# Kernel optimization log

Hardware: AMD Instinct MI355X
Metric: run time of the kernel (lower is better)

The kernel has to match this reference:

```python
import jax, jax.numpy as jnp
import numpy as np

N, DIM = 8192, 128
NEG = -1e9  # finite stand-in for -inf; exp underflows to 0 for masked entries


def setup_inputs() -> dict:
    key = jax.random.key(0)
    k1, k2, k3, k4 = jax.random.split(key, 4)
    h = jax.random.normal(k1, (N, DIM), dtype=jnp.float32)
    social_adj = jax.random.randint(k2, (N, N), 0, 2, dtype=jnp.int32)
    # nn.Linear(dim, dim, bias=False): weight [out, in]; xavier-ish scale
    W = jax.random.normal(k3, (DIM, DIM), dtype=jnp.float32) / np.sqrt(DIM)
    a = jax.random.normal(k4, (2 * DIM,), dtype=jnp.float32) / np.sqrt(2 * DIM)
    return {"h": h, "social_adj": social_adj, "W": W, "a": a}


def reference(h, social_adj, W, a):
    Wh = h @ W.T                              # [N, d]
    d = Wh.shape[1]
    a1 = Wh @ a[:d]                           # [N]
    a2 = Wh @ a[d:]                           # [N]
    e = jax.nn.leaky_relu(a1[:, None] + a2[None, :], negative_slope=0.2)  # [N, N]
    mask = social_adj != 0
    e = jnp.where(mask, e, NEG)
    alpha = jax.nn.softmax(e, axis=-1)        # [N, N]
    # rows with no neighbors: torch gives nan->0 via nan_to_num; we zero them directly
    no_neighbor = ~jnp.any(mask, axis=-1)     # [N]
    alpha = jnp.where(no_neighbor[:, None], 0.0, alpha)
    out = alpha @ Wh                          # [N, d]; already 0 on no_neighbor rows
    return out, alpha
```

## Files before the change

### kernel.cpp

```cpp
#include <hip/hip_runtime.h>
#include <hip/hip_bf16.h>

#define NN 8192
#define DIM 128
#define KS 8
#define KSL (NN / KS)
#define RPB 64
#define KC 128

typedef __attribute__((ext_vector_type(8))) short bf16x8;
typedef __attribute__((ext_vector_type(4))) float f32x4;
typedef __attribute__((ext_vector_type(4))) int i32x4;
typedef __attribute__((ext_vector_type(4))) unsigned int u32x4;
typedef __attribute__((ext_vector_type(4))) unsigned short u16x4;
typedef __attribute__((ext_vector_type(4))) short s16x4;

static __device__ inline unsigned short f2bf(float x) {
    __hip_bfloat16 b = __float2bfloat16(x);
    return *reinterpret_cast<unsigned short*>(&b);
}

struct BSplit { short hi, lo; };
static __device__ inline BSplit bsplit(float x) {
    BSplit r;
    __hip_bfloat16 h = __float2bfloat16(x);
    r.hi = *reinterpret_cast<short*>(&h);
    float rem = x - __bfloat162float(h);
    __hip_bfloat16 l = __float2bfloat16(rem);
    r.lo = *reinterpret_cast<short*>(&l);
    return r;
}

__global__ __launch_bounds__(256) void k1m(const float* __restrict__ h,
                                           const float* __restrict__ W,
                                           const float* __restrict__ a,
                                           __hip_bfloat16* __restrict__ whbT,
                                           float* __restrict__ a1g,
                                           unsigned* __restrict__ pku) {
    __shared__ short whi[128 * 132];
    __shared__ short wlo[128 * 132];
    __shared__ short wt[8 * 128 * 8];
    __shared__ float a_sh[256];

    const int tid = threadIdx.x;
    const int wv = tid >> 6, lane = tid & 63;
    const int r0 = blockIdx.x * 64;

    for (int idx = tid; idx < 128 * 128; idx += 256) {
        const int d = idx >> 7, k = idx & 127;
        BSplit s = bsplit(W[idx]);
        whi[d * 132 + k] = s.hi;
        wlo[d * 132 + k] = s.lo;
    }
    a_sh[tid] = a[tid];
    __syncthreads();

    f32x4 acc[8];
    #pragma unroll
    for (int n = 0; n < 8; ++n) acc[n] = (f32x4){0.f, 0.f, 0.f, 0.f};

    const int arow = r0 + wv * 16 + (lane & 15);
    const int ksub = (lane >> 4) * 8;
    const float* hp = h + (size_t)arow * DIM + ksub;

    #pragma unroll
    for (int kk = 0; kk < 128; kk += 32) {
        f32x4 x0 = *(const f32x4*)(hp + kk);
        f32x4 x1 = *(const f32x4*)(hp + kk + 4);
        bf16x8 ah, al;
        {
            BSplit s0 = bsplit(x0.x), s1 = bsplit(x0.y), s2 = bsplit(x0.z), s3 = bsplit(x0.w);
            BSplit s4 = bsplit(x1.x), s5 = bsplit(x1.y), s6 = bsplit(x1.z), s7 = bsplit(x1.w);
            ah[0] = s0.hi; al[0] = s0.lo; ah[1] = s1.hi; al[1] = s1.lo;
            ah[2] = s2.hi; al[2] = s2.lo; ah[3] = s3.hi; al[3] = s3.lo;
            ah[4] = s4.hi; al[4] = s4.lo; ah[5] = s5.hi; al[5] = s5.lo;
            ah[6] = s6.hi; al[6] = s6.lo; ah[7] = s7.hi; al[7] = s7.lo;
        }
        #pragma unroll
        for (int n = 0; n < 8; ++n) {
            const int boff = (n * 16 + (lane & 15)) * 132 + kk + ksub;
            bf16x8 bh = *(const bf16x8*)(whi + boff);
            bf16x8 bl = *(const bf16x8*)(wlo + boff);
            acc[n] = __builtin_amdgcn_mfma_f32_16x16x32_bf16(ah, bh, acc[n], 0, 0, 0);
            acc[n] = __builtin_amdgcn_mfma_f32_16x16x32_bf16(ah, bl, acc[n], 0, 0, 0);
            acc[n] = __builtin_amdgcn_mfma_f32_16x16x32_bf16(al, bh, acc[n], 0, 0, 0);
        }
    }

    float p1[4] = {0.f, 0.f, 0.f, 0.f}, p2[4] = {0.f, 0.f, 0.f, 0.f};
    #pragma unroll
    for (int n = 0; n < 8; ++n) {
        const float av1 = a_sh[n * 16 + (lane & 15)];
        const float av2 = a_sh[128 + n * 16 + (lane & 15)];
        #pragma unroll
        for (int q = 0; q < 4; ++q) {
            p1[q] += acc[n][q] * av1;
            p2[q] += acc[n][q] * av2;
        }
    }
    #pragma unroll
    for (int o = 8; o >= 1; o >>= 1) {
        #pragma unroll
        for (int q = 0; q < 4; ++q) {
            p1[q] += __shfl_xor(p1[q], o, 64);
            p2[q] += __shfl_xor(p2[q], o, 64);
        }
    }
    if ((lane & 15) == 0) {
        #pragma unroll
        for (int q = 0; q < 4; ++q) {
            const int row = r0 + wv * 16 + (lane >> 4) * 4 + q;
            a1g[row] = p1[q];
            const float E1v = expf(p2[q]);
            const float E2v = expf(0.2f * p2[q]);
            pku[row] = (unsigned)f2bf(E1v) | ((unsigned)f2bf(E2v) << 16);
        }
    }

    #pragma unroll
    for (int n = 0; n < 8; ++n) {
        #pragma unroll
        for (int q = 0; q < 4; ++q) {
            const int kloc = wv * 16 + (lane >> 4) * 4 + q;
            const int d = n * 16 + (lane & 15);
            wt[(kloc >> 3) * 1024 + d * 8 + (kloc & 7)] = (short)f2bf(acc[n][q]);
        }
    }
    __syncthreads();
    short* dst = reinterpret_cast<short*>(whbT) + ((size_t)r0 << 7);
    for (int idx = tid * 4; idx < 8192; idx += 1024)
        *(s16x4*)(dst + idx) = *(const s16x4*)(wt + idx);
}

static __device__ inline void sa_group(const i32x4 v, const u32x4 tb,
                                       const float T, const int lane,
                                       float& s1, float& s2,
                                       unsigned* __restrict__ bgrp) {
    unsigned long long m0 = __ballot(v.x != 0);
    unsigned long long m1 = __ballot(v.y != 0);
    unsigned long long m2 = __ballot(v.z != 0);
    unsigned long long m3 = __ballot(v.w != 0);
    if (lane == 0) {
        u32x4 w;
        w.x = (unsigned)m0; w.y = (unsigned)m1;
        w.z = (unsigned)m2; w.w = (unsigned)m3;
        *(u32x4*)(bgrp) = w;
    } else if (lane == 32) {
        u32x4 w;
        w.x = (unsigned)(m0 >> 32); w.y = (unsigned)(m1 >> 32);
        w.z = (unsigned)(m2 >> 32); w.w = (unsigned)(m3 >> 32);
        *(u32x4*)(bgrp + 4) = w;
    }
    float e1, e2; bool px;
    e1 = __uint_as_float(tb.x << 16); e2 = __uint_as_float(tb.x & 0xffff0000u);
    px = (e1 >= T);
    s1 += (v.x && px) ? e1 : 0.f;  s2 += (v.x && !px) ? e2 : 0.f;
    e1 = __uint_as_float(tb.y << 16); e2 = __uint_as_float(tb.y & 0xffff0000u);
    px = (e1 >= T);
    s1 += (v.y && px) ? e1 : 0.f;  s2 += (v.y && !px) ? e2 : 0.f;
    e1 = __uint_as_float(tb.z << 16); e2 = __uint_as_float(tb.z & 0xffff0000u);
    px = (e1 >= T);
    s1 += (v.z && px) ? e1 : 0.f;  s2 += (v.z && !px) ? e2 : 0.f;
    e1 = __uint_as_float(tb.w << 16); e2 = __uint_as_float(tb.w & 0xffff0000u);
    px = (e1 >= T);
    s1 += (v.w && px) ? e1 : 0.f;  s2 += (v.w && !px) ? e2 : 0.f;
}

__global__ __launch_bounds__(256) void sa_scan(const int* __restrict__ adj,
                                               const float* __restrict__ a1g,
                                               const unsigned* __restrict__ pku,
                                               unsigned* __restrict__ bm,
                                               float* __restrict__ crow) {
    const int wid = threadIdx.x >> 6, lane = threadIdx.x & 63;
    const int i = blockIdx.x * 4 + wid;
    const float a1i = a1g[i];
    const float T = expf(-a1i);
    const int* arow = adj + (size_t)i * NN;
    unsigned* brow = bm + (size_t)i * (NN / 32);

    float s1 = 0.f, s2 = 0.f;
    for (int it = 0; it < NN / 1024; ++it) {
        const int j0 = it * 1024 + lane * 4;
        i32x4 v0 = __builtin_nontemporal_load((const i32x4*)(arow + j0));
        i32x4 v1 = __builtin_nontemporal_load((const i32x4*)(arow + j0 + 256));
        i32x4 v2 = __builtin_nontemporal_load((const i32x4*)(arow + j0 + 512));
        i32x4 v3 = __builtin_nontemporal_load((const i32x4*)(arow + j0 + 768));
        u32x4 t0 = *(const u32x4*)(pku + j0);
        u32x4 t1 = *(const u32x4*)(pku + j0 + 256);
        u32x4 t2 = *(const u32x4*)(pku + j0 + 512);
        u32x4 t3 = *(const u32x4*)(pku + j0 + 768);
        unsigned* bsup = brow + it * 32;
        sa_group(v0, t0, T, lane, s1, s2, bsup);
        sa_group(v1, t1, T, lane, s1, s2, bsup + 8);
        sa_group(v2, t2, T, lane, s1, s2, bsup + 16);
        sa_group(v3, t3, T, lane, s1, s2, bsup + 24);
    }
    #pragma unroll
    for (int o = 32; o >= 1; o >>= 1) {
        s1 += __shfl_xor(s1, o, 64);
        s2 += __shfl_xor(s2, o, 64);
    }
    if (lane == 0) {
        float c1 = 0.f, c2 = 0.f;
        if (s1 + s2 > 0.f) {
            float e1v = expf(a1i);
            float e2v = expf(0.2f * a1i);
            float S = e1v * s1 + e2v * s2;
            c1 = e1v / S;
            c2 = e2v / S;
        }
        crow[i * 4 + 0] = c1;
        crow[i * 4 + 1] = c2;
        crow[i * 4 + 2] = T;
        crow[i * 4 + 3] = 0.f;
    }
}

__global__ __launch_bounds__(512, 8) void sb_pv(const unsigned* __restrict__ bm,
                                                const float* __restrict__ crowG,
                                                const unsigned* __restrict__ pku,
                                                const __hip_bfloat16* __restrict__ whbT,
                                                float* __restrict__ alpha,
                                                float* __restrict__ part) {
    __shared__ __hip_bfloat16 abuf[2][RPB][KC + 8];

    const int tid = threadIdx.x;
    const int wv = tid >> 6, lane = tid & 63;
    const int r0 = blockIdx.x * RPB;
    const int ks = blockIdx.y;
    const int k0 = ks * KSL;

    const int rloc = tid >> 5;
    float c1r[4], c2r[4], Tr[4];
    #pragma unroll
    for (int v = 0; v < 4; ++v) {
        f32x4 cw = *(const f32x4*)(crowG + (size_t)(r0 + rloc + 16 * v) * 4);
        c1r[v] = cw.x; c2r[v] = cw.y; Tr[v] = cw.z;
    }

    f32x4 acc[4];
    #pragma unroll
    for (int rt = 0; rt < 4; ++rt) acc[rt] = (f32x4){0.f, 0.f, 0.f, 0.f};
    const int n0 = wv * 16;
    const short* wb = reinterpret_cast<const short*>(whbT);
    const short* bbase = wb + (size_t)(n0 + (lane & 15)) * 8 + (size_t)(lane >> 4) * 1024;

    const int cgrp = (tid & 31) << 2;
    const unsigned pbit = tid & 31;

    for (int kc = 0; kc < KSL; kc += KC) {
        const int dbuf = (kc >> 7) & 1;
        const int jl = kc + cgrp;
        const int j = k0 + jl;
        const int wbw = ((jl >> 8) << 3) + (((jl >> 7) & 1) << 2);
        u32x4 tb = *(const u32x4*)(pku + j);
        float e1c[4], e2c[4];
        e1c[0] = __uint_as_float(tb.x << 16); e2c[0] = __uint_as_float(tb.x & 0xffff0000u);
        e1c[1] = __uint_as_float(tb.y << 16); e2c[1] = __uint_as_float(tb.y & 0xffff0000u);
        e1c[2] = __uint_as_float(tb.z << 16); e2c[2] = __uint_as_float(tb.z & 0xffff0000u);
        e1c[3] = __uint_as_float(tb.w << 16); e2c[3] = __uint_as_float(tb.w & 0xffff0000u);
        #pragma unroll
        for (int v = 0; v < 4; ++v) {
            const int r = rloc + 16 * v;
            const int gr = r0 + r;
            u32x4 w4 = *(const u32x4*)(bm + (size_t)gr * (NN / 32) + ks * (KSL / 32) + wbw);
            const float c1 = c1r[v], c2 = c2r[v], T = Tr[v];
            f32x4 al;
            al.x = ((w4.x >> pbit) & 1) ? ((e1c[0] >= T) ? c1 * e1c[0] : c2 * e2c[0]) : 0.f;
            al.y = ((w4.y >> pbit) & 1) ? ((e1c[1] >= T) ? c1 * e1c[1] : c2 * e2c[1]) : 0.f;
            al.z = ((w4.z >> pbit) & 1) ? ((e1c[2] >= T) ? c1 * e1c[2] : c2 * e2c[2]) : 0.f;
            al.w = ((w4.w >> pbit) & 1) ? ((e1c[3] >= T) ? c1 * e1c[3] : c2 * e2c[3]) : 0.f;
            __builtin_nontemporal_store(al, (f32x4*)(alpha + (size_t)gr * NN + j));
            u16x4 ub4;
            ub4.x = f2bf(al.x); ub4.y = f2bf(al.y); ub4.z = f2bf(al.z); ub4.w = f2bf(al.w);
            *(u16x4*)(&abuf[dbuf][r][cgrp]) = ub4;
        }
        __syncthreads();
        #pragma unroll
        for (int kk = 0; kk < KC; kk += 32) {
            bf16x8 bf = *(const bf16x8*)(bbase + (size_t)((k0 + kc + kk) >> 3) * 1024);
            #pragma unroll
            for (int rt = 0; rt < 4; ++rt) {
                bf16x8 af = *(const bf16x8*)(&abuf[dbuf][rt * 16 + (lane & 15)][kk + 8 * (lane >> 4)]);
                acc[rt] = __builtin_amdgcn_mfma_f32_16x16x32_bf16(af, bf, acc[rt], 0, 0, 0);
            }
        }
    }

    float* pb2 = part + (size_t)ks * NN * DIM;
    const int rb = (lane >> 4) * 4;
    #pragma unroll
    for (int rt = 0; rt < 4; ++rt) {
        #pragma unroll
        for (int q = 0; q < 4; ++q)
            pb2[(size_t)(r0 + rt * 16 + rb + q) * DIM + n0 + (lane & 15)] = acc[rt][q];
    }
}

__global__ __launch_bounds__(256) void k5_reduce(const float* __restrict__ part,
                                                 float* __restrict__ out) {
    const size_t idx = ((size_t)blockIdx.x * 256 + threadIdx.x) * 4;
    f32x4 s = (f32x4){0.f, 0.f, 0.f, 0.f};
    #pragma unroll
    for (int ks = 0; ks < KS; ++ks)
        s += *(const f32x4*)(part + (size_t)ks * NN * DIM + idx);
    *(f32x4*)(out + idx) = s;
}

extern "C" void kernel_launch(void* const* d_in, const int* in_sizes, int n_in,
                              void* d_out, int out_size, void* d_ws, size_t ws_size,
                              hipStream_t stream) {
    const float* h   = (const float*)d_in[0];
    const int*   adj = (const int*)d_in[1];
    const float* W   = (const float*)d_in[2];
    const float* a   = (const float*)d_in[3];

    float* out   = (float*)d_out;
    float* alpha = out + (size_t)NN * DIM;

    char* ws = (char*)d_ws;
    __hip_bfloat16* whbT = (__hip_bfloat16*)(ws);
    float* a1g    = (float*)(ws + 0x200000);
    unsigned* pku = (unsigned*)(ws + 0x208000);
    float* crow   = (float*)(ws + 0x218000);
    unsigned* bm  = (unsigned*)(ws + 0x240000);
    float* part   = (float*)(ws + 0xA40000);

    k1m<<<NN / 64, 256, 0, stream>>>(h, W, a, whbT, a1g, pku);
    sa_scan<<<NN / 4, 256, 0, stream>>>(adj, a1g, pku, bm, crow);
    sb_pv<<<dim3(NN / RPB, KS), 512, 0, stream>>>(bm, crow, pku, whbT, alpha, part);
    k5_reduce<<<NN * DIM / 1024, 256, 0, stream>>>(part, out);
}
```

Measured before the change: 161.5 us.

## Fuse mask scan, alpha generation and PV matmul into one kernel per 8 rows

Merges the adjacency scan, alpha write/PV MFMA and split-K reduction kernels into a single kernel where each block handles 8 rows. The block keeps the row bitmask and softmax constants in shared memory and accumulates the full K range itself. This removes the global bitmask round trip, the partial-sum buffer and the reduce kernel. In exchange, half of each 16-row MFMA tile is zero padding, so matrix-core work per useful row doubles. Each Wh tile is also reused by only 8 rows, which raises Wh traffic from L2.

```diff
diff --git a/kernel.cpp b/kernel.cpp
--- a/kernel.cpp
+++ b/kernel.cpp
@@ -3,10 +3,8 @@
 
 #define NN 8192
 #define DIM 128
-#define KS 8
-#define KSL (NN / KS)
-#define RPB 64
-#define KC 128
+#define RPB 8
+#define KC 256
 
 typedef __attribute__((ext_vector_type(8))) short bf16x8;
 typedef __attribute__((ext_vector_type(4))) float f32x4;
@@ -135,7 +133,7 @@
 static __device__ inline void sa_group(const i32x4 v, const u32x4 tb,
                                        const float T, const int lane,
                                        float& s1, float& s2,
-                                       unsigned* __restrict__ bgrp) {
+                                       unsigned* bgrp) {
     unsigned long long m0 = __ballot(v.x != 0);
     unsigned long long m1 = __ballot(v.y != 0);
     unsigned long long m2 = __ballot(v.z != 0);
@@ -166,145 +164,103 @@
     s1 += (v.w && px) ? e1 : 0.f;  s2 += (v.w && !px) ? e2 : 0.f;
 }
 
-__global__ __launch_bounds__(256) void sa_scan(const int* __restrict__ adj,
-                                               const float* __restrict__ a1g,
-                                               const unsigned* __restrict__ pku,
-                                               unsigned* __restrict__ bm,
-                                               float* __restrict__ crow) {
-    const int wid = threadIdx.x >> 6, lane = threadIdx.x & 63;
-    const int i = blockIdx.x * 4 + wid;
-    const float a1i = a1g[i];
-    const float T = expf(-a1i);
-    const int* arow = adj + (size_t)i * NN;
-    unsigned* brow = bm + (size_t)i * (NN / 32);
-
-    float s1 = 0.f, s2 = 0.f;
-    for (int it = 0; it < NN / 1024; ++it) {
-        const int j0 = it * 1024 + lane * 4;
-        i32x4 v0 = __builtin_nontemporal_load((const i32x4*)(arow + j0));
-        i32x4 v1 = __builtin_nontemporal_load((const i32x4*)(arow + j0 + 256));
-        i32x4 v2 = __builtin_nontemporal_load((const i32x4*)(arow + j0 + 512));
-        i32x4 v3 = __builtin_nontemporal_load((const i32x4*)(arow + j0 + 768));
-        u32x4 t0 = *(const u32x4*)(pku + j0);
-        u32x4 t1 = *(const u32x4*)(pku + j0 + 256);
-        u32x4 t2 = *(const u32x4*)(pku + j0 + 512);
-        u32x4 t3 = *(const u32x4*)(pku + j0 + 768);
-        unsigned* bsup = brow + it * 32;
-        sa_group(v0, t0, T, lane, s1, s2, bsup);
-        sa_group(v1, t1, T, lane, s1, s2, bsup + 8);
-        sa_group(v2, t2, T, lane, s1, s2, bsup + 16);
-        sa_group(v3, t3, T, lane, s1, s2, bsup + 24);
-    }
-    #pragma unroll
-    for (int o = 32; o >= 1; o >>= 1) {
-        s1 += __shfl_xor(s1, o, 64);
-        s2 += __shfl_xor(s2, o, 64);
-    }
-    if (lane == 0) {
-        float c1 = 0.f, c2 = 0.f;
-        if (s1 + s2 > 0.f) {
-            float e1v = expf(a1i);
-            float e2v = expf(0.2f * a1i);
-            float S = e1v * s1 + e2v * s2;
-            c1 = e1v / S;
-            c2 = e2v / S;
-        }
-        crow[i * 4 + 0] = c1;
-        crow[i * 4 + 1] = c2;
-        crow[i * 4 + 2] = T;
-        crow[i * 4 + 3] = 0.f;
-    }
-}
-
-__global__ __launch_bounds__(512, 8) void sb_pv(const unsigned* __restrict__ bm,
-                                                const float* __restrict__ crowG,
-                                                const unsigned* __restrict__ pku,
-                                                const __hip_bfloat16* __restrict__ whbT,
-                                                float* __restrict__ alpha,
-                                                float* __restrict__ part) {
-    __shared__ __hip_bfloat16 abuf[2][RPB][KC + 8];
+__global__ __launch_bounds__(512, 8) void fs(const int* __restrict__ adj,
+                                             const float* __restrict__ a1g,
+                                             const unsigned* __restrict__ pku,
+                                             const __hip_bfloat16* __restrict__ whbT,
+                                             float* __restrict__ alpha,
+                                             float* __restrict__ out) {
+    __shared__ unsigned bmL[RPB][256];
+    __shared__ __hip_bfloat16 abuf[2][16][KC + 8];
+    __shared__ float crowL[RPB][4];
 
     const int tid = threadIdx.x;
     const int wv = tid >> 6, lane = tid & 63;
     const int r0 = blockIdx.x * RPB;
-    const int ks = blockIdx.y;
-    const int k0 = ks * KSL;
-
-    const int rloc = tid >> 5;
-    float c1r[4], c2r[4], Tr[4];
-    #pragma unroll
-    for (int v = 0; v < 4; ++v) {
-        f32x4 cw = *(const f32x4*)(crowG + (size_t)(r0 + rloc + 16 * v) * 4);
-        c1r[v] = cw.x; c2r[v] = cw.y; Tr[v] = cw.z;
-    }
-
-    f32x4 acc[4];
-    #pragma unroll
-    for (int rt = 0; rt < 4; ++rt) acc[rt] = (f32x4){0.f, 0.f, 0.f, 0.f};
+
+    #pragma unroll
+    for (int b = 0; b < 2; ++b) {
+        unsigned* pz = (unsigned*)&abuf[b][8][0];
+        for (int idx = tid; idx < 4 * (KC + 8); idx += 512) pz[idx] = 0;
+    }
+
+    {
+        const int gi = r0 + wv;
+        const float a1i = a1g[gi];
+        const float T = expf(-a1i);
+        const int* arow = adj + (size_t)gi * NN;
+        float s1 = 0.f, s2 = 0.f;
+        for (int it = 0; it < NN / 512; ++it) {
+            const int j0 = it * 512 + lane * 4;
+            i32x4 v0 = __builtin_nontemporal_load((const i32x4*)(arow + j0));
+            i32x4 v1 = __builtin_nontemporal_load((const i32x4*)(arow + j0 + 256));
+            u32x4 t0 = *(const u32x4*)(pku + j0);
+            u32x4 t1 = *(const u32x4*)(pku + j0 + 256);
+            sa_group(v0, t0, T, lane, s1, s2, &bmL[wv][it * 16]);
+            sa_group(v1, t1, T, lane, s1, s2, &bmL[wv][it * 16 + 8]);
+        }
+        #pragma unroll
+        for (int o = 32; o >= 1; o >>= 1) {
+            s1 += __shfl_xor(s1, o, 64);
+            s2 += __shfl_xor(s2, o, 64);
+        }
+        if (lane == 0) {
+            float c1 = 0.f, c2 = 0.f;
+            if (s1 + s2 > 0.f) {
+                float e1v = expf(a1i);
+                float e2v = expf(0.2f * a1i);
+                float S = e1v * s1 + e2v * s2;
+                c1 = e1v / S;
+                c2 = e2v / S;
+            }
+            crowL[wv][0] = c1; crowL[wv][1] = c2; crowL[wv][2] = T;
+        }
+    }
+    __syncthreads();
+
+    const float c1 = crowL[wv][0], c2 = crowL[wv][1], Tb = crowL[wv][2];
+    f32x4 acc = (f32x4){0.f, 0.f, 0.f, 0.f};
     const int n0 = wv * 16;
     const short* wb = reinterpret_cast<const short*>(whbT);
     const short* bbase = wb + (size_t)(n0 + (lane & 15)) * 8 + (size_t)(lane >> 4) * 1024;
-
-    const int cgrp = (tid & 31) << 2;
-    const unsigned pbit = tid & 31;
-
-    for (int kc = 0; kc < KSL; kc += KC) {
-        const int dbuf = (kc >> 7) & 1;
-        const int jl = kc + cgrp;
-        const int j = k0 + jl;
-        const int wbw = ((jl >> 8) << 3) + (((jl >> 7) & 1) << 2);
+    float* arow_out = alpha + (size_t)(r0 + wv) * NN;
+    const unsigned pbit = lane & 31;
+
+    for (int kc = 0; kc < NN; kc += KC) {
+        const int dbuf = (kc >> 8) & 1;
+        const int j = kc + lane * 4;
+        const int wbw = ((j >> 8) << 3) + (((j >> 7) & 1) << 2);
         u32x4 tb = *(const u32x4*)(pku + j);
+        u32x4 w4 = *(const u32x4*)(&bmL[wv][wbw]);
         float e1c[4], e2c[4];
         e1c[0] = __uint_as_float(tb.x << 16); e2c[0] = __uint_as_float(tb.x & 0xffff0000u);
         e1c[1] = __uint_as_float(tb.y << 16); e2c[1] = __uint_as_float(tb.y & 0xffff0000u);
         e1c[2] = __uint_as_float(tb.z << 16); e2c[2] = __uint_as_float(tb.z & 0xffff0000u);
         e1c[3] = __uint_as_float(tb.w << 16); e2c[3] = __uint_as_float(tb.w & 0xffff0000u);
-        #pragma unroll
-        for (int v = 0; v < 4; ++v) {
-            const int r = rloc + 16 * v;
-            const int gr = r0 + r;
-            u32x4 w4 = *(const u32x4*)(bm + (size_t)gr * (NN / 32) + ks * (KSL / 32) + wbw);
-            const float c1 = c1r[v], c2 = c2r[v], T = Tr[v];
-            f32x4 al;
-            al.x = ((w4.x >> pbit) & 1) ? ((e1c[0] >= T) ? c1 * e1c[0] : c2 * e2c[0]) : 0.f;
-            al.y = ((w4.y >> pbit) & 1) ? ((e1c[1] >= T) ? c1 * e1c[1] : c2 * e2c[1]) : 0.f;
-            al.z = ((w4.z >> pbit) & 1) ? ((e1c[2] >= T) ? c1 * e1c[2] : c2 * e2c[2]) : 0.f;
-            al.w = ((w4.w >> pbit) & 1) ? ((e1c[3] >= T) ? c1 * e1c[3] : c2 * e2c[3]) : 0.f;
-            __builtin_nontemporal_store(al, (f32x4*)(alpha + (size_t)gr * NN + j));
-            u16x4 ub4;
-            ub4.x = f2bf(al.x); ub4.y = f2bf(al.y); ub4.z = f2bf(al.z); ub4.w = f2bf(al.w);
-            *(u16x4*)(&abuf[dbuf][r][cgrp]) = ub4;
-        }
+        f32x4 al;
+        al.x = ((w4.x >> pbit) & 1) ? ((e1c[0] >= Tb) ? c1 * e1c[0] : c2 * e2c[0]) : 0.f;
+        al.y = ((w4.y >> pbit) & 1) ? ((e1c[1] >= Tb) ? c1 * e1c[1] : c2 * e2c[1]) : 0.f;
+        al.z = ((w4.z >> pbit) & 1) ? ((e1c[2] >= Tb) ? c1 * e1c[2] : c2 * e2c[2]) : 0.f;
+        al.w = ((w4.w >> pbit) & 1) ? ((e1c[3] >= Tb) ? c1 * e1c[3] : c2 * e2c[3]) : 0.f;
+        __builtin_nontemporal_store(al, (f32x4*)(arow_out + j));
+        u16x4 ub4;
+        ub4.x = f2bf(al.x); ub4.y = f2bf(al.y); ub4.z = f2bf(al.z); ub4.w = f2bf(al.w);
+        *(u16x4*)(&abuf[dbuf][wv][lane * 4]) = ub4;
         __syncthreads();
         #pragma unroll
         for (int kk = 0; kk < KC; kk += 32) {
-            bf16x8 bf = *(const bf16x8*)(bbase + (size_t)((k0 + kc + kk) >> 3) * 1024);
-            #pragma unroll
-            for (int rt = 0; rt < 4; ++rt) {
-                bf16x8 af = *(const bf16x8*)(&abuf[dbuf][rt * 16 + (lane & 15)][kk + 8 * (lane >> 4)]);
-                acc[rt] = __builtin_amdgcn_mfma_f32_16x16x32_bf16(af, bf, acc[rt], 0, 0, 0);
-            }
-        }
-    }
-
-    float* pb2 = part + (size_t)ks * NN * DIM;
-    const int rb = (lane >> 4) * 4;
-    #pragma unroll
-    for (int rt = 0; rt < 4; ++rt) {
+            bf16x8 bf = *(const bf16x8*)(bbase + (size_t)((kc + kk) >> 3) * 1024);
+            bf16x8 af = *(const bf16x8*)(&abuf[dbuf][lane & 15][kk + 8 * (lane >> 4)]);
+            acc = __builtin_amdgcn_mfma_f32_16x16x32_bf16(af, bf, acc, 0, 0, 0);
+        }
+    }
+
+    const int rl = (lane >> 4) * 4;
+    if (rl < RPB) {
         #pragma unroll
         for (int q = 0; q < 4; ++q)
-            pb2[(size_t)(r0 + rt * 16 + rb + q) * DIM + n0 + (lane & 15)] = acc[rt][q];
-    }
-}
-
-__global__ __launch_bounds__(256) void k5_reduce(const float* __restrict__ part,
-                                                 float* __restrict__ out) {
-    const size_t idx = ((size_t)blockIdx.x * 256 + threadIdx.x) * 4;
-    f32x4 s = (f32x4){0.f, 0.f, 0.f, 0.f};
-    #pragma unroll
-    for (int ks = 0; ks < KS; ++ks)
-        s += *(const f32x4*)(part + (size_t)ks * NN * DIM + idx);
-    *(f32x4*)(out + idx) = s;
+            out[(size_t)(r0 + rl + q) * DIM + n0 + (lane & 15)] = acc[q];
+    }
 }
 
 extern "C" void kernel_launch(void* const* d_in, const int* in_sizes, int n_in,
@@ -322,12 +278,7 @@
     __hip_bfloat16* whbT = (__hip_bfloat16*)(ws);
     float* a1g    = (float*)(ws + 0x200000);
     unsigned* pku = (unsigned*)(ws + 0x208000);
-    float* crow   = (float*)(ws + 0x218000);
-    unsigned* bm  = (unsigned*)(ws + 0x240000);
-    float* part   = (float*)(ws + 0xA40000);
 
     k1m<<<NN / 64, 256, 0, stream>>>(h, W, a, whbT, a1g, pku);
-    sa_scan<<<NN / 4, 256, 0, stream>>>(adj, a1g, pku, bm, crow);
-    sb_pv<<<dim3(NN / RPB, KS), 512, 0, stream>>>(bm, crow, pku, whbT, alpha, part);
-    k5_reduce<<<NN * DIM / 1024, 256, 0, stream>>>(part, out);
-}
+    fs<<<NN / RPB, 512, 0, stream>>>(adj, a1g, pku, whbT, alpha, out);
+}
```

After: 161.5 us. Within noise of the previous version (-0.0%).
